# Performance work log

Measured on AMD Instinct MI355X. Metric: run time of the kernel, lower is better.

## Reference

```python
import jax, jax.numpy as jnp
import numpy as np

B, S, H = 32, 2048, 4096   # requests, tokens per request, hidden
R = 64                      # adapter out_features (LoRA-rank-like)
N_ADAPTERS = 16


def setup_inputs() -> dict:
    key = jax.random.key(0)
    k1, k2, k3 = jax.random.split(key, 3)
    x = jax.random.normal(k1, (B, S, H), dtype=jnp.float32)
    adapter_ids = jax.random.randint(k2, (B,), 0, N_ADAPTERS)
    # learned per-adapter weights, F.linear layout [out, in]
    weight = jax.random.normal(k3, (N_ADAPTERS, R, H), dtype=jnp.float32) * 0.02
    return {"x": x, "adapter_ids": adapter_ids, "weight": weight}


def reference(x, adapter_ids, weight):
    # Original: for each sample i, _forward(x[i], weight[adapter_ids][i])
    # where _forward is a linear: y = x @ w.T. Vectorized as a gathered
    # batched GEMM instead of the Python loop.
    w = weight[adapter_ids]                      # [B, R, H] per-sample weight gather
    return jnp.einsum('bsh,brh->bsr', x, w)      # [B, S, R]
```

## Files before the change

kernel.cpp:

```cpp
#include <hip/hip_runtime.h>

#define B_  32
#define S_  2048
#define H_  4096
#define R_  64

typedef __attribute__((ext_vector_type(8))) short  bf16x8;
typedef __attribute__((ext_vector_type(4))) float  f32x4;

__device__ __forceinline__ unsigned pkbf(float a, float b) {
    unsigned ua = __builtin_bit_cast(unsigned, a) + 0x8000u;
    unsigned ub = __builtin_bit_cast(unsigned, b) + 0x8000u;
    return (ua >> 16) | (ub & 0xFFFF0000u);
}

__device__ __forceinline__ bf16x8 cvt8(f32x4 lo, f32x4 hi) {
    union { unsigned u[4]; bf16x8 v; } r;
    r.u[0] = pkbf(lo[0], lo[1]);
    r.u[1] = pkbf(lo[2], lo[3]);
    r.u[2] = pkbf(hi[0], hi[1]);
    r.u[3] = pkbf(hi[2], hi[3]);
    return r.v;
}

__global__ __launch_bounds__(64, 1) void multilora_mfma(
        const float* __restrict__ x,
        const int*   __restrict__ ids,
        const float* __restrict__ w,
        float*       __restrict__ out) {
    const int lane = threadIdx.x;
    const int blk  = blockIdx.x;
    const int b    = blk >> 5;
    const int s0   = (blk & 31) << 6;
    const int a    = ids[b];

    const int l15  = lane & 15;
    const int quad = lane >> 4;
    const int koff = quad * 8;

    const float* xbase = x + ((size_t)b * S_ + s0) * H_ + koff;
    const float* wbase = w + ((size_t)a * R_) * H_ + koff;

    const float* ax[4];
    const float* bw[4];
#pragma unroll
    for (int i = 0; i < 4; ++i) {
        ax[i] = xbase + (size_t)(i * 16 + l15) * H_;
        bw[i] = wbase + (size_t)(i * 16 + l15) * H_;
    }

    f32x4 acc[4][4];
#pragma unroll
    for (int mi = 0; mi < 4; ++mi)
#pragma unroll
        for (int ni = 0; ni < 4; ++ni)
            acc[mi][ni] = (f32x4){0.f, 0.f, 0.f, 0.f};

    f32x4 xa[4][2], xb[4][2];
#pragma unroll
    for (int i = 0; i < 4; ++i) {
        xa[i][0] = *(const f32x4*)(ax[i]);
        xa[i][1] = *(const f32x4*)(ax[i] + 4);
        xb[i][0] = *(const f32x4*)(bw[i]);
        xb[i][1] = *(const f32x4*)(bw[i] + 4);
        ax[i] += 32; bw[i] += 32;
    }

    for (int k = 0; k < H_; k += 32) {
        bf16x8 af[4], bfr[4];
#pragma unroll
        for (int i = 0; i < 4; ++i) {
            af[i]  = cvt8(xa[i][0], xa[i][1]);
            bfr[i] = cvt8(xb[i][0], xb[i][1]);
        }
        if (k + 32 < H_) {
#pragma unroll
            for (int i = 0; i < 4; ++i) {
                xa[i][0] = *(const f32x4*)(ax[i]);
                xa[i][1] = *(const f32x4*)(ax[i] + 4);
                xb[i][0] = *(const f32x4*)(bw[i]);
                xb[i][1] = *(const f32x4*)(bw[i] + 4);
                ax[i] += 32; bw[i] += 32;
            }
        }
#pragma unroll
        for (int mi = 0; mi < 4; ++mi)
#pragma unroll
            for (int ni = 0; ni < 4; ++ni)
                acc[mi][ni] = __builtin_amdgcn_mfma_f32_16x16x32_bf16(
                    af[mi], bfr[ni], acc[mi][ni], 0, 0, 0);
    }

    float* ob = out + ((size_t)b * S_ + s0) * R_ + l15;
#pragma unroll
    for (int mi = 0; mi < 4; ++mi) {
#pragma unroll
        for (int i = 0; i < 4; ++i) {
            const int row = mi * 16 + quad * 4 + i;
            float* p = ob + (size_t)row * R_;
#pragma unroll
            for (int ni = 0; ni < 4; ++ni)
                p[ni * 16] = acc[mi][ni][i];
        }
    }
}

extern "C" void kernel_launch(void* const* d_in, const int* in_sizes, int n_in,
                              void* d_out, int out_size, void* d_ws, size_t ws_size,
                              hipStream_t stream) {
    const float* x   = (const float*)d_in[0];
    const int*   ids = (const int*)d_in[1];
    const float* w   = (const float*)d_in[2];
    float*       out = (float*)d_out;

    const int grid = B_ * (S_ / 64);
    multilora_mfma<<<grid, 64, 0, stream>>>(x, ids, w, out);
}
```

Measured before the change: 1.389 ms.

## Split 64-row tile across four waves with deeper prefetch and block swizzle

Each block now runs four waves, each computing a 16-row slice of the 64x64 output tile against all 64 adapter columns, instead of a single wave doing the whole tile. The K loop is unrolled by two with staged prefetch of x and weight fragments, and block indices are permuted across eight groups. The aim is more resident waves per CU to hide global-load latency in this bandwidth-bound GEMM. In exchange, every wave reloads the full weight slice, which raises cache traffic for weights.

New measurement: 1.662 ms. +19.7%, slower.

```diff
diff --git a/kernel.cpp b/kernel.cpp
--- a/kernel.cpp
+++ b/kernel.cpp
@@ -23,85 +23,100 @@
     return r.v;
 }
 
-__global__ __launch_bounds__(64, 1) void multilora_mfma(
+__global__ __launch_bounds__(256, 4) void multilora_mfma(
         const float* __restrict__ x,
         const int*   __restrict__ ids,
         const float* __restrict__ w,
         float*       __restrict__ out) {
-    const int lane = threadIdx.x;
-    const int blk  = blockIdx.x;
-    const int b    = blk >> 5;
-    const int s0   = (blk & 31) << 6;
-    const int a    = ids[b];
+    const int nblk = B_ * (S_ / 64);
+    const int raw  = blockIdx.x;
+    const int blk  = (raw & 7) * (nblk >> 3) + (raw >> 3);
 
+    const int b   = blk >> 5;
+    const int s0  = (blk & 31) << 6;
+    const int a   = ids[b];
+
+    const int wid  = threadIdx.x >> 6;
+    const int lane = threadIdx.x & 63;
     const int l15  = lane & 15;
     const int quad = lane >> 4;
-    const int koff = quad * 8;
 
-    const float* xbase = x + ((size_t)b * S_ + s0) * H_ + koff;
-    const float* wbase = w + ((size_t)a * R_) * H_ + koff;
+    const float* ap = x + ((size_t)b * S_ + s0 + wid * 16 + l15) * H_ + quad * 8;
+    const float* wp0;
+    const float* wp1;
+    const float* wp2;
+    const float* wp3;
+    {
+        const float* wbase = w + ((size_t)a * R_ + l15) * H_ + quad * 8;
+        wp0 = wbase;
+        wp1 = wbase + (size_t)16 * H_;
+        wp2 = wbase + (size_t)32 * H_;
+        wp3 = wbase + (size_t)48 * H_;
+    }
 
-    const float* ax[4];
-    const float* bw[4];
+    f32x4 acc[4];
+#pragma unroll
+    for (int i = 0; i < 4; ++i) acc[i] = (f32x4){0.f, 0.f, 0.f, 0.f};
+
+    f32x4 xA0, xA1, xB0, xB1;
+    f32x4 ws[4][2];
+
+    xA0 = *(const f32x4*)(ap);
+    xA1 = *(const f32x4*)(ap + 4);
+    xB0 = *(const f32x4*)(ap + 32);
+    xB1 = *(const f32x4*)(ap + 36);
+    ws[0][0] = *(const f32x4*)(wp0);  ws[0][1] = *(const f32x4*)(wp0 + 4);
+    ws[1][0] = *(const f32x4*)(wp1);  ws[1][1] = *(const f32x4*)(wp1 + 4);
+    ws[2][0] = *(const f32x4*)(wp2);  ws[2][1] = *(const f32x4*)(wp2 + 4);
+    ws[3][0] = *(const f32x4*)(wp3);  ws[3][1] = *(const f32x4*)(wp3 + 4);
+
+    for (int k = 0; k < H_; k += 64) {
+        bf16x8 bfr[4];
+#pragma unroll
+        for (int i = 0; i < 4; ++i) bfr[i] = cvt8(ws[i][0], ws[i][1]);
+        if (k + 32 < H_) {
+            ws[0][0] = *(const f32x4*)(wp0 + 32);  ws[0][1] = *(const f32x4*)(wp0 + 36);
+            ws[1][0] = *(const f32x4*)(wp1 + 32);  ws[1][1] = *(const f32x4*)(wp1 + 36);
+            ws[2][0] = *(const f32x4*)(wp2 + 32);  ws[2][1] = *(const f32x4*)(wp2 + 36);
+            ws[3][0] = *(const f32x4*)(wp3 + 32);  ws[3][1] = *(const f32x4*)(wp3 + 36);
+        }
+        bf16x8 af = cvt8(xA0, xA1);
+        if (k + 64 < H_) {
+            xA0 = *(const f32x4*)(ap + 64);
+            xA1 = *(const f32x4*)(ap + 68);
+        }
+#pragma unroll
+        for (int i = 0; i < 4; ++i)
+            acc[i] = __builtin_amdgcn_mfma_f32_16x16x32_bf16(af, bfr[i], acc[i], 0, 0, 0);
+
+#pragma unroll
+        for (int i = 0; i < 4; ++i) bfr[i] = cvt8(ws[i][0], ws[i][1]);
+        if (k + 64 < H_) {
+            ws[0][0] = *(const f32x4*)(wp0 + 64);  ws[0][1] = *(const f32x4*)(wp0 + 68);
+            ws[1][0] = *(const f32x4*)(wp1 + 64);  ws[1][1] = *(const f32x4*)(wp1 + 68);
+            ws[2][0] = *(const f32x4*)(wp2 + 64);  ws[2][1] = *(const f32x4*)(wp2 + 68);
+            ws[3][0] = *(const f32x4*)(wp3 + 64);  ws[3][1] = *(const f32x4*)(wp3 + 68);
+        }
+        af = cvt8(xB0, xB1);
+        if (k + 96 < H_) {
+            xB0 = *(const f32x4*)(ap + 96);
+            xB1 = *(const f32x4*)(ap + 100);
+        }
+#pragma unroll
+        for (int i = 0; i < 4; ++i)
+            acc[i] = __builtin_amdgcn_mfma_f32_16x16x32_bf16(af, bfr[i], acc[i], 0, 0, 0);
+
+        ap += 64;
+        wp0 += 64; wp1 += 64; wp2 += 64; wp3 += 64;
+    }
+
+    float* ob = out + ((size_t)b * S_ + s0 + wid * 16) * R_ + l15;
 #pragma unroll
     for (int i = 0; i < 4; ++i) {
-        ax[i] = xbase + (size_t)(i * 16 + l15) * H_;
-        bw[i] = wbase + (size_t)(i * 16 + l15) * H_;
-    }
-
-    f32x4 acc[4][4];
-#pragma unroll
-    for (int mi = 0; mi < 4; ++mi)
+        float* p = ob + (size_t)(quad * 4 + i) * R_;
 #pragma unroll
         for (int ni = 0; ni < 4; ++ni)
-            acc[mi][ni] = (f32x4){0.f, 0.f, 0.f, 0.f};
-
-    f32x4 xa[4][2], xb[4][2];
-#pragma unroll
-    for (int i = 0; i < 4; ++i) {
-        xa[i][0] = *(const f32x4*)(ax[i]);
-        xa[i][1] = *(const f32x4*)(ax[i] + 4);
-        xb[i][0] = *(const f32x4*)(bw[i]);
-        xb[i][1] = *(const f32x4*)(bw[i] + 4);
-        ax[i] += 32; bw[i] += 32;
-    }
-
-    for (int k = 0; k < H_; k += 32) {
-        bf16x8 af[4], bfr[4];
-#pragma unroll
-        for (int i = 0; i < 4; ++i) {
-            af[i]  = cvt8(xa[i][0], xa[i][1]);
-            bfr[i] = cvt8(xb[i][0], xb[i][1]);
-        }
-        if (k + 32 < H_) {
-#pragma unroll
-            for (int i = 0; i < 4; ++i) {
-                xa[i][0] = *(const f32x4*)(ax[i]);
-                xa[i][1] = *(const f32x4*)(ax[i] + 4);
-                xb[i][0] = *(const f32x4*)(bw[i]);
-                xb[i][1] = *(const f32x4*)(bw[i] + 4);
-                ax[i] += 32; bw[i] += 32;
-            }
-        }
-#pragma unroll
-        for (int mi = 0; mi < 4; ++mi)
-#pragma unroll
-            for (int ni = 0; ni < 4; ++ni)
-                acc[mi][ni] = __builtin_amdgcn_mfma_f32_16x16x32_bf16(
-                    af[mi], bfr[ni], acc[mi][ni], 0, 0, 0);
-    }
-
-    float* ob = out + ((size_t)b * S_ + s0) * R_ + l15;
-#pragma unroll
-    for (int mi = 0; mi < 4; ++mi) {
-#pragma unroll
-        for (int i = 0; i < 4; ++i) {
-            const int row = mi * 16 + quad * 4 + i;
-            float* p = ob + (size_t)row * R_;
-#pragma unroll
-            for (int ni = 0; ni < 4; ++ni)
-                p[ni * 16] = acc[mi][ni][i];
-        }
+            p[ni * 16] = acc[ni][i];
     }
 }
 
@@ -114,5 +129,5 @@
     float*       out = (float*)d_out;
 
     const int grid = B_ * (S_ / 64);
-    multilora_mfma<<<grid, 64, 0, stream>>>(x, ids, w, out);
+    multilora_mfma<<<grid, 256, 0, stream>>>(x, ids, w, out);
 }
```

## Share adapter weights via LDS across 8 waves with double-buffered k-steps

Applied to the files above, without the earlier changes.

Replaces the single-wave 64x64 tile kernel with a 512-thread block covering 128 rows. Each wave computes 16 rows against all 64 adapter outputs. The adapter weight tile is converted to bf16 once per block and staged in a double-buffered LDS array, so weight global reads are shared by all waves instead of being reloaded per wave. It also remaps block indices to group blocks with the same batch, adds register prefetch of x two k-steps ahead, and synchronises with a barrier every k-step, which may add stall overhead.

Result: faster. 1.338 ms (-3.7%).

```diff
diff --git a/kernel.cpp b/kernel.cpp
--- a/kernel.cpp
+++ b/kernel.cpp
@@ -4,6 +4,7 @@
 #define S_  2048
 #define H_  4096
 #define R_  64
+#define NT  64
 
 typedef __attribute__((ext_vector_type(8))) short  bf16x8;
 typedef __attribute__((ext_vector_type(4))) float  f32x4;
@@ -23,85 +24,138 @@
     return r.v;
 }
 
-__global__ __launch_bounds__(64, 1) void multilora_mfma(
+__global__ __launch_bounds__(512, 4) void multilora_mfma(
         const float* __restrict__ x,
         const int*   __restrict__ ids,
         const float* __restrict__ w,
         float*       __restrict__ out) {
-    const int lane = threadIdx.x;
-    const int blk  = blockIdx.x;
-    const int b    = blk >> 5;
-    const int s0   = (blk & 31) << 6;
-    const int a    = ids[b];
+    __shared__ bf16x8 lw[2][512];
 
+    const int raw = blockIdx.x;
+    const int blk = (raw & 7) * 64 + (raw >> 3);
+    const int b   = blk >> 4;
+    const int s0  = (blk & 15) << 7;
+    const int a   = ids[b];
+
+    const int tid  = threadIdx.x;
+    const int wid  = tid >> 6;
+    const int lane = tid & 63;
     const int l15  = lane & 15;
     const int quad = lane >> 4;
-    const int koff = quad * 8;
 
-    const float* xbase = x + ((size_t)b * S_ + s0) * H_ + koff;
-    const float* wbase = w + ((size_t)a * R_) * H_ + koff;
+    const float* ap = x + ((size_t)b * S_ + s0 + wid * 16 + l15) * H_ + quad * 8;
+    const float* wp = w + ((size_t)a * R_ + lane) * H_ + wid * 8;
+    const int slot_w = ((wid >> 2) * 4 + (lane >> 4)) * 64 + (wid & 3) * 16 + l15;
 
-    const float* ax[4];
-    const float* bw[4];
+    f32x4 acc[4];
+#pragma unroll
+    for (int i = 0; i < 4; ++i) acc[i] = (f32x4){0.f, 0.f, 0.f, 0.f};
+
+    f32x4 xA[4], xB[4], wg0, wg1;
+    xA[0] = *(const f32x4*)(ap);
+    xA[1] = *(const f32x4*)(ap + 4);
+    xA[2] = *(const f32x4*)(ap + 32);
+    xA[3] = *(const f32x4*)(ap + 36);
+    xB[0] = *(const f32x4*)(ap + 64);
+    xB[1] = *(const f32x4*)(ap + 68);
+    xB[2] = *(const f32x4*)(ap + 96);
+    xB[3] = *(const f32x4*)(ap + 100);
+    wg0 = *(const f32x4*)(wp);
+    wg1 = *(const f32x4*)(wp + 4);
+    lw[0][slot_w] = cvt8(wg0, wg1);
+    wg0 = *(const f32x4*)(wp + 64);
+    wg1 = *(const f32x4*)(wp + 68);
+    asm volatile("s_waitcnt lgkmcnt(0)" ::: "memory");
+    __builtin_amdgcn_s_barrier();
+    __builtin_amdgcn_sched_barrier(0);
+
+    for (int tt = 0; tt < 31; ++tt) {
+        {
+            bf16x8 a0 = cvt8(xA[0], xA[1]);
+            bf16x8 a1 = cvt8(xA[2], xA[3]);
+            const float* p = ap + (size_t)(2 * tt + 2) * 64;
+            xA[0] = *(const f32x4*)(p);
+            xA[1] = *(const f32x4*)(p + 4);
+            xA[2] = *(const f32x4*)(p + 32);
+            xA[3] = *(const f32x4*)(p + 36);
+#pragma unroll
+            for (int ni = 0; ni < 4; ++ni)
+                acc[ni] = __builtin_amdgcn_mfma_f32_16x16x32_bf16(
+                    a0, lw[0][ni * 64 + lane], acc[ni], 0, 0, 0);
+#pragma unroll
+            for (int ni = 0; ni < 4; ++ni)
+                acc[ni] = __builtin_amdgcn_mfma_f32_16x16x32_bf16(
+                    a1, lw[0][256 + ni * 64 + lane], acc[ni], 0, 0, 0);
+            lw[1][slot_w] = cvt8(wg0, wg1);
+            const float* q = wp + (size_t)(2 * tt + 2) * 64;
+            wg0 = *(const f32x4*)(q);
+            wg1 = *(const f32x4*)(q + 4);
+            asm volatile("s_waitcnt lgkmcnt(0)" ::: "memory");
+            __builtin_amdgcn_s_barrier();
+            __builtin_amdgcn_sched_barrier(0);
+        }
+        {
+            bf16x8 a0 = cvt8(xB[0], xB[1]);
+            bf16x8 a1 = cvt8(xB[2], xB[3]);
+            const float* p = ap + (size_t)(2 * tt + 3) * 64;
+            xB[0] = *(const f32x4*)(p);
+            xB[1] = *(const f32x4*)(p + 4);
+            xB[2] = *(const f32x4*)(p + 32);
+            xB[3] = *(const f32x4*)(p + 36);
+#pragma unroll
+            for (int ni = 0; ni < 4; ++ni)
+                acc[ni] = __builtin_amdgcn_mfma_f32_16x16x32_bf16(
+                    a0, lw[1][ni * 64 + lane], acc[ni], 0, 0, 0);
+#pragma unroll
+            for (int ni = 0; ni < 4; ++ni)
+                acc[ni] = __builtin_amdgcn_mfma_f32_16x16x32_bf16(
+                    a1, lw[1][256 + ni * 64 + lane], acc[ni], 0, 0, 0);
+            lw[0][slot_w] = cvt8(wg0, wg1);
+            const float* q = wp + (size_t)(2 * tt + 3) * 64;
+            wg0 = *(const f32x4*)(q);
+            wg1 = *(const f32x4*)(q + 4);
+            asm volatile("s_waitcnt lgkmcnt(0)" ::: "memory");
+            __builtin_amdgcn_s_barrier();
+            __builtin_amdgcn_sched_barrier(0);
+        }
+    }
+
+    {
+        bf16x8 a0 = cvt8(xA[0], xA[1]);
+        bf16x8 a1 = cvt8(xA[2], xA[3]);
+#pragma unroll
+        for (int ni = 0; ni < 4; ++ni)
+            acc[ni] = __builtin_amdgcn_mfma_f32_16x16x32_bf16(
+                a0, lw[0][ni * 64 + lane], acc[ni], 0, 0, 0);
+#pragma unroll
+        for (int ni = 0; ni < 4; ++ni)
+            acc[ni] = __builtin_amdgcn_mfma_f32_16x16x32_bf16(
+                a1, lw[0][256 + ni * 64 + lane], acc[ni], 0, 0, 0);
+        lw[1][slot_w] = cvt8(wg0, wg1);
+        asm volatile("s_waitcnt lgkmcnt(0)" ::: "memory");
+        __builtin_amdgcn_s_barrier();
+        __builtin_amdgcn_sched_barrier(0);
+    }
+    {
+        bf16x8 a0 = cvt8(xB[0], xB[1]);
+        bf16x8 a1 = cvt8(xB[2], xB[3]);
+#pragma unroll
+        for (int ni = 0; ni < 4; ++ni)
+            acc[ni] = __builtin_amdgcn_mfma_f32_16x16x32_bf16(
+                a0, lw[1][ni * 64 + lane], acc[ni], 0, 0, 0);
+#pragma unroll
+        for (int ni = 0; ni < 4; ++ni)
+            acc[ni] = __builtin_amdgcn_mfma_f32_16x16x32_bf16(
+                a1, lw[1][256 + ni * 64 + lane], acc[ni], 0, 0, 0);
+    }
+
+    float* ob = out + ((size_t)b * S_ + s0 + wid * 16) * R_ + l15;
 #pragma unroll
     for (int i = 0; i < 4; ++i) {
-        ax[i] = xbase + (size_t)(i * 16 + l15) * H_;
-        bw[i] = wbase + (size_t)(i * 16 + l15) * H_;
-    }
-
-    f32x4 acc[4][4];
-#pragma unroll
-    for (int mi = 0; mi < 4; ++mi)
+        float* prow = ob + (size_t)(quad * 4 + i) * R_;
 #pragma unroll
         for (int ni = 0; ni < 4; ++ni)
-            acc[mi][ni] = (f32x4){0.f, 0.f, 0.f, 0.f};
-
-    f32x4 xa[4][2], xb[4][2];
-#pragma unroll
-    for (int i = 0; i < 4; ++i) {
-        xa[i][0] = *(const f32x4*)(ax[i]);
-        xa[i][1] = *(const f32x4*)(ax[i] + 4);
-        xb[i][0] = *(const f32x4*)(bw[i]);
-        xb[i][1] = *(const f32x4*)(bw[i] + 4);
-        ax[i] += 32; bw[i] += 32;
-    }
-
-    for (int k = 0; k < H_; k += 32) {
-        bf16x8 af[4], bfr[4];
-#pragma unroll
-        for (int i = 0; i < 4; ++i) {
-            af[i]  = cvt8(xa[i][0], xa[i][1]);
-            bfr[i] = cvt8(xb[i][0], xb[i][1]);
-        }
-        if (k + 32 < H_) {
-#pragma unroll
-            for (int i = 0; i < 4; ++i) {
-                xa[i][0] = *(const f32x4*)(ax[i]);
-                xa[i][1] = *(const f32x4*)(ax[i] + 4);
-                xb[i][0] = *(const f32x4*)(bw[i]);
-                xb[i][1] = *(const f32x4*)(bw[i] + 4);
-                ax[i] += 32; bw[i] += 32;
-            }
-        }
-#pragma unroll
-        for (int mi = 0; mi < 4; ++mi)
-#pragma unroll
-            for (int ni = 0; ni < 4; ++ni)
-                acc[mi][ni] = __builtin_amdgcn_mfma_f32_16x16x32_bf16(
-                    af[mi], bfr[ni], acc[mi][ni], 0, 0, 0);
-    }
-
-    float* ob = out + ((size_t)b * S_ + s0) * R_ + l15;
-#pragma unroll
-    for (int mi = 0; mi < 4; ++mi) {
-#pragma unroll
-        for (int i = 0; i < 4; ++i) {
-            const int row = mi * 16 + quad * 4 + i;
-            float* p = ob + (size_t)row * R_;
-#pragma unroll
-            for (int ni = 0; ni < 4; ++ni)
-                p[ni * 16] = acc[mi][ni][i];
-        }
+            prow[ni * 16] = acc[ni][i];
     }
 }
 
@@ -113,6 +167,6 @@
     const float* w   = (const float*)d_in[2];
     float*       out = (float*)d_out;
 
-    const int grid = B_ * (S_ / 64);
-    multilora_mfma<<<grid, 64, 0, stream>>>(x, ids, w, out);
+    const int grid = B_ * (S_ / 128);
+    multilora_mfma<<<grid, 512, 0, stream>>>(x, ids, w, out);
 }
```
